# Kernel optimization log

Hardware: AMD Instinct MI355X
Metric: run time of the kernel (lower is better)

The kernel has to match this reference:

```python
import jax, jax.numpy as jnp
import numpy as np

EPS = 1e-15
B, N_PER, D, K, DEG = 64, 1024, 256, 64, 16  # graphs, nodes/graph, feat dim, pools/graph, avg degree


def setup_inputs() -> dict:
    key = jax.random.key(0)
    k1, k2, k3, k4 = jax.random.split(key, 4)
    N = B * N_PER
    E = B * N_PER * DEG
    x = jax.random.normal(k1, (N, D), jnp.float32)
    # edges confined within each graph (block-diagonal batched adjacency)
    rng = np.random.default_rng(0)
    offs = np.repeat(np.arange(B, dtype=np.int64) * N_PER, N_PER * DEG)
    src = rng.integers(0, N_PER, size=E) + offs
    dst = rng.integers(0, N_PER, size=E) + offs
    edge_index = jnp.asarray(np.stack([src, dst], axis=0), dtype=jnp.int32)
    edge_weight = jax.random.uniform(k2, (E,), jnp.float32)
    batch_ptr = jnp.arange(B + 1, dtype=jnp.int32) * N_PER
    W = jax.random.normal(k3, (D, K), jnp.float32) * 0.05  # pooling_net = Linear(D, K)
    b = jnp.zeros((K,), jnp.float32)
    gumbel_noise = jax.random.gumbel(k4, (N, K), jnp.float32)
    return {"x": x, "edge_weight": edge_weight, "W": W, "b": b,
            "gumbel_noise": gumbel_noise, "edge_index": edge_index, "batch_ptr": batch_ptr}


def _stochpool(x, edge_weight, W, b, gumbel_noise, edge_index, batch_ptr):
    N, Dd = x.shape
    nb = batch_ptr.shape[0] - 1          # num graphs
    n = N // nb                          # nodes per graph (equal-sized graphs)
    E = edge_index.shape[1]
    e_per = E // nb                      # edges per graph

    # pooling net + hard gumbel softmax (straight-through, tau=1)
    logits = x @ W + b                   # (N, K)
    y_soft = jax.nn.softmax(logits + gumbel_noise, axis=-1)
    y_hard = jax.nn.one_hot(jnp.argmax(y_soft, axis=-1), W.shape[1], dtype=y_soft.dtype)
    s = jax.lax.stop_gradient(y_hard - y_soft) + y_soft   # (N, K)

    u, v = edge_index[0], edge_index[1]
    graph_of_edge = u // n               # (E,) graph id per edge

    s_b = s.reshape(nb, n, -1)           # (B, n, K)
    x_b = x.reshape(nb, n, Dd)

    # pooled features: s^T x per graph
    out = jnp.einsum('bnk,bnd->bkd', s_b, x_b).reshape(nb * s_b.shape[2], Dd)

    # pooled adjacency: s^T A s per graph, via As = scatter-add over edges
    As = jnp.zeros_like(s).at[u].add(edge_weight[:, None] * s[v])   # (N, K) : (A s)
    out_adj = jnp.einsum('bnk,bnl->bkl', s_b, As.reshape(nb, n, -1))  # (B, K, K)

    # link loss: ||A - S S^T||_F per graph, via Frobenius expansion (no n x n dense)
    sq_A = jax.ops.segment_sum(edge_weight * edge_weight, graph_of_edge, num_segments=nb)
    cross = jax.ops.segment_sum(edge_weight * jnp.sum(s[u] * s[v], axis=-1),
                                graph_of_edge, num_segments=nb)
    StS = jnp.einsum('bnk,bnl->bkl', s_b, s_b)                # (B, K, K)
    sq_SSt = jnp.sum(StS * StS, axis=(1, 2))                  # ||S S^T||_F^2 = ||S^T S||_F^2
    link = jnp.sqrt(jnp.maximum(sq_A - 2.0 * cross + sq_SSt, 0.0))
    link = link / e_per                                       # normalize=True
    link_loss = jnp.mean(link)

    entropy_loss = jnp.mean(jnp.sum(-s * jnp.log(s + EPS), axis=-1))

    Kp = s_b.shape[2]
    batch = jnp.repeat(jnp.arange(nb, dtype=jnp.int32), Kp)
    batch_ptr_out = jnp.arange(0, (nb + 1) * Kp, Kp, dtype=jnp.int32)
    return out, out_adj, link_loss, entropy_loss, batch, batch_ptr_out


def reference(x, edge_weight, W, b, gumbel_noise, edge_index, batch_ptr):
    return _stochpool(x, edge_weight, W, b, gumbel_noise, edge_index, batch_ptr)
```

## Files before the change

### kernel.cpp

```cpp
#include <hip/hip_runtime.h>

#define NN 65536
#define DD 256
#define KK 64
#define NPG 1024

#define OUT_OFF   0
#define ADJ_OFF   1048576
#define LINK_OFF  1310720
#define ENT_OFF   1310721
#define BATCH_OFF 1310722
#define BPTR_OFF  1314818

#define WS_ASSIGN 0
#define WS_S1     262144
#define WS_C      524288
#define WS_SQP    540672
#define WS_CRP    541696
#define WS_ENTP   542720
#define WS_SORT   1048576
#define WS_GOFF   1310720
#define WS_ADJP   1331200
#define WS_NEED   (WS_ADJP + 256 * 4096 * 4)

typedef __bf16 bf16x8 __attribute__((ext_vector_type(8)));
typedef unsigned short u16x8 __attribute__((ext_vector_type(8)));
typedef float f32x4 __attribute__((ext_vector_type(4)));

static __device__ __forceinline__ unsigned short f2bf(float f) {
  unsigned int u = __float_as_uint(f);
  return (unsigned short)((u + 0x7fffu + ((u >> 16) & 1u)) >> 16);
}

__global__ __launch_bounds__(256, 4) void pool_assign_kernel(
    const float* __restrict__ x, const float* __restrict__ Wm,
    const float* __restrict__ bvec, const float* __restrict__ gum,
    int* __restrict__ assign, float* __restrict__ s1g,
    float* __restrict__ entp)
{
  __shared__ unsigned short lds_wt[64 * 264];
  __shared__ float esum[4];
  const int t    = threadIdx.x;
  const int lane = t & 63;
  const int wv   = t >> 6;
  const int q    = lane >> 4;
  const int c    = lane & 15;
  const int nb0  = blockIdx.x << 6;

  #pragma unroll 8
  for (int i = 0; i < 64; ++i) {
    int idx = (i << 8) + t;
    lds_wt[(idx & 63) * 264 + (idx >> 6)] = f2bf(Wm[idx]);
  }

  const int arow = nb0 + (wv << 4) + c;
  const float* xrow = x + (size_t)arow * DD + (q << 3);
  u16x8 afr[8];
  #pragma unroll
  for (int kb = 0; kb < 8; ++kb) {
    float4 u0 = *(const float4*)(xrow + kb * 32);
    float4 u1 = *(const float4*)(xrow + kb * 32 + 4);
    u16x8 af;
    af[0] = f2bf(u0.x); af[1] = f2bf(u0.y); af[2] = f2bf(u0.z); af[3] = f2bf(u0.w);
    af[4] = f2bf(u1.x); af[5] = f2bf(u1.y); af[6] = f2bf(u1.z); af[7] = f2bf(u1.w);
    afr[kb] = af;
  }
  __syncthreads();

  f32x4 acc[4];
  #pragma unroll
  for (int n = 0; n < 4; ++n) acc[n] = (f32x4){0.f, 0.f, 0.f, 0.f};
  #pragma unroll
  for (int n = 0; n < 4; ++n) {
    #pragma unroll
    for (int kb = 0; kb < 8; ++kb) {
      u16x8 bu = *(const u16x8*)(&lds_wt[(n * 16 + c) * 264 + kb * 32 + (q << 3)]);
      acc[n] = __builtin_amdgcn_mfma_f32_16x16x32_bf16(
          __builtin_bit_cast(bf16x8, afr[kb]),
          __builtin_bit_cast(bf16x8, bu), acc[n], 0, 0, 0);
    }
  }

  float bb[4];
  #pragma unroll
  for (int n = 0; n < 4; ++n) bb[n] = bvec[n * 16 + c];
  const int nodeq = nb0 + (wv << 4) + (q << 2);
  float ent = 0.f;
  #pragma unroll
  for (int reg = 0; reg < 4; ++reg) {
    float zz[4];
    #pragma unroll
    for (int n = 0; n < 4; ++n)
      zz[n] = acc[n][reg] + bb[n] + gum[(size_t)(nodeq + reg) * KK + n * 16 + c];
    float m = zz[0]; int a = c;
    #pragma unroll
    for (int n = 1; n < 4; ++n)
      if (zz[n] > m) { m = zz[n]; a = n * 16 + c; }
    #pragma unroll
    for (int mask = 1; mask <= 8; mask <<= 1) {
      float mo = __shfl_xor(m, mask, 64);
      int   ao = __shfl_xor(a, mask, 64);
      if (mo > m || (mo == m && ao < a)) { m = mo; a = ao; }
    }
    float ls = 0.f;
    #pragma unroll
    for (int n = 0; n < 4; ++n) ls += expf(zz[n] - m);
    #pragma unroll
    for (int mask = 1; mask <= 8; mask <<= 1) ls += __shfl_xor(ls, mask, 64);
    if (c == 0) {
      int node = nodeq + reg;
      float p  = 1.0f / ls;
      float s1 = (1.0f - p) + p;
      assign[node] = a;
      s1g[node]    = s1;
      ent += -s1 * logf(s1 + 1e-15f);
    }
  }
  #pragma unroll
  for (int off = 32; off; off >>= 1) ent += __shfl_down(ent, off, 64);
  if (lane == 0) esum[wv] = ent;
  __syncthreads();
  if (t == 0) entp[blockIdx.x] = esum[0] + esum[1] + esum[2] + esum[3];
}

__global__ __launch_bounds__(256) void sort_kernel(
    const int* __restrict__ assign, const float* __restrict__ s1,
    int* __restrict__ sorted, int* __restrict__ goff,
    float* __restrict__ c_out)
{
  __shared__ int hist[64];
  __shared__ int offs[65];
  __shared__ int cursor[64];
  const int t = threadIdx.x;
  const int g = blockIdx.x;
  const int n0 = g << 10;
  if (t < 64) hist[t] = 0;
  __syncthreads();
  int4 av = ((const int4*)(assign + n0))[t];
  atomicAdd(&hist[av.x], 1);
  atomicAdd(&hist[av.y], 1);
  atomicAdd(&hist[av.z], 1);
  atomicAdd(&hist[av.w], 1);
  __syncthreads();
  if (t == 0) {
    int s = 0;
    #pragma unroll
    for (int k = 0; k < 64; ++k) { offs[k] = s; s += hist[k]; }
    offs[64] = s;
  }
  __syncthreads();
  if (t < 64) cursor[t] = offs[t];
  if (t < 65) goff[g * 65 + t] = offs[t];
  __syncthreads();
  int p;
  p = atomicAdd(&cursor[av.x], 1); sorted[n0 + p] = n0 + t * 4 + 0;
  p = atomicAdd(&cursor[av.y], 1); sorted[n0 + p] = n0 + t * 4 + 1;
  p = atomicAdd(&cursor[av.z], 1); sorted[n0 + p] = n0 + t * 4 + 2;
  p = atomicAdd(&cursor[av.w], 1); sorted[n0 + p] = n0 + t * 4 + 3;
  __syncthreads();
  if (t < 64) {
    float cs = 0.f;
    int e = offs[t + 1];
    for (int o = offs[t]; o < e; ++o) {
      float v = s1[sorted[n0 + o]];
      cs += v * v;
    }
    c_out[(g << 6) + t] = cs;
  }
}

__global__ __launch_bounds__(256, 8) void gather_kernel(
    const float* __restrict__ x, const float* __restrict__ s1,
    const int* __restrict__ sorted, const int* __restrict__ goff,
    float* __restrict__ out)
{
  const int t = threadIdx.x;
  const int g = blockIdx.x >> 6;
  const int k = blockIdx.x & 63;
  const int o0 = goff[g * 65 + k];
  const int o1 = goff[g * 65 + k + 1];
  const int* sp = sorted + (g << 10);
  float sum = 0.f;
  int i = o0;
  for (; i + 4 <= o1; i += 4) {
    int n0 = sp[i], n1 = sp[i + 1], n2 = sp[i + 2], n3 = sp[i + 3];
    float w0 = s1[n0], w1 = s1[n1], w2 = s1[n2], w3 = s1[n3];
    float x0 = x[(size_t)n0 * DD + t];
    float x1 = x[(size_t)n1 * DD + t];
    float x2 = x[(size_t)n2 * DD + t];
    float x3 = x[(size_t)n3 * DD + t];
    sum += w0 * x0 + w1 * x1 + w2 * x2 + w3 * x3;
  }
  for (; i < o1; ++i) {
    int n = sp[i];
    sum += s1[n] * x[(size_t)n * DD + t];
  }
  out[((size_t)(g * 64 + k)) * DD + t] = sum;
}

__global__ __launch_bounds__(1024, 2) void edge_kernel(
    const int* __restrict__ src, const int* __restrict__ dst,
    const float* __restrict__ ew, const int* __restrict__ assign,
    const float* __restrict__ s1, float* __restrict__ adj_partial,
    float* __restrict__ sqP, float* __restrict__ crP)
{
  __shared__ float adj[4096];
  __shared__ float redsq[16], redcr[16];
  const int t   = threadIdx.x;
  const int blk = blockIdx.x;
  const int g   = blk >> 2;
  #pragma unroll
  for (int i = 0; i < 4; ++i) adj[i * 1024 + t] = 0.f;
  __syncthreads();
  const int e0 = (g << 14) + ((blk & 3) << 12);
  float sq = 0.f, cr = 0.f;
  #pragma unroll
  for (int i = 0; i < 4; ++i) {
    int e = e0 + i * 1024 + t;
    int u = src[e], v = dst[e];
    float w = ew[e];
    int au = assign[u], av = assign[v];
    float contrib = w * s1[u] * s1[v];
    atomicAdd(&adj[au * 64 + av], contrib);
    sq += w * w;
    if (au == av) cr += contrib;
  }
  #pragma unroll
  for (int off = 32; off; off >>= 1) {
    sq += __shfl_down(sq, off, 64);
    cr += __shfl_down(cr, off, 64);
  }
  if ((t & 63) == 0) { redsq[t >> 6] = sq; redcr[t >> 6] = cr; }
  __syncthreads();
  if (t == 0) {
    float a = 0.f, b2 = 0.f;
    #pragma unroll
    for (int i = 0; i < 16; ++i) { a += redsq[i]; b2 += redcr[i]; }
    sqP[blk] = a;
    crP[blk] = b2;
  }
  float* pp = adj_partial + (size_t)blk * 4096;
  #pragma unroll
  for (int i = 0; i < 4; ++i) pp[i * 1024 + t] = adj[i * 1024 + t];
}

__global__ __launch_bounds__(1024) void adj_combine_kernel(
    const float* __restrict__ adj_partial, float* __restrict__ out_adj)
{
  int idx = blockIdx.x * 1024 + threadIdx.x;
  int g = idx >> 12;
  int cell = idx & 4095;
  const float* p = adj_partial + ((size_t)(g * 4)) * 4096 + cell;
  out_adj[idx] = p[0] + p[4096] + p[8192] + p[12288];
}

__global__ __launch_bounds__(1024, 2) void edge_kernel_atomic(
    const int* __restrict__ src, const int* __restrict__ dst,
    const float* __restrict__ ew, const int* __restrict__ assign,
    const float* __restrict__ s1, float* __restrict__ out_adj,
    float* __restrict__ sqP, float* __restrict__ crP)
{
  __shared__ float adj[4096];
  __shared__ float redsq[16], redcr[16];
  const int t   = threadIdx.x;
  const int blk = blockIdx.x;
  const int g   = blk >> 2;
  #pragma unroll
  for (int i = 0; i < 4; ++i) adj[i * 1024 + t] = 0.f;
  __syncthreads();
  const int e0 = (g << 14) + ((blk & 3) << 12);
  float sq = 0.f, cr = 0.f;
  #pragma unroll
  for (int i = 0; i < 4; ++i) {
    int e = e0 + i * 1024 + t;
    int u = src[e], v = dst[e];
    float w = ew[e];
    int au = assign[u], av = assign[v];
    float contrib = w * s1[u] * s1[v];
    atomicAdd(&adj[au * 64 + av], contrib);
    sq += w * w;
    if (au == av) cr += contrib;
  }
  #pragma unroll
  for (int off = 32; off; off >>= 1) {
    sq += __shfl_down(sq, off, 64);
    cr += __shfl_down(cr, off, 64);
  }
  if ((t & 63) == 0) { redsq[t >> 6] = sq; redcr[t >> 6] = cr; }
  __syncthreads();
  if (t == 0) {
    float a = 0.f, b2 = 0.f;
    #pragma unroll
    for (int i = 0; i < 16; ++i) { a += redsq[i]; b2 += redcr[i]; }
    sqP[blk] = a;
    crP[blk] = b2;
  }
  float* adjg = out_adj + (size_t)g * 4096;
  #pragma unroll
  for (int i = 0; i < 4; ++i)
    atomicAdd(&adjg[i * 1024 + t], adj[i * 1024 + t]);
}

__global__ __launch_bounds__(256) void finalize_kernel(
    const float* __restrict__ c, const float* __restrict__ sqP,
    const float* __restrict__ crP, const float* __restrict__ entp,
    float* __restrict__ out)
{
  __shared__ float esum2[4];
  const int t = threadIdx.x;
  float link = 0.f;
  if (t < 64) {
    const float* cg = c + t * 64;
    float ssq = 0.f;
    #pragma unroll
    for (int k = 0; k < 64; ++k) ssq += cg[k] * cg[k];
    float sq = sqP[4 * t] + sqP[4 * t + 1] + sqP[4 * t + 2] + sqP[4 * t + 3];
    float cr = crP[4 * t] + crP[4 * t + 1] + crP[4 * t + 2] + crP[4 * t + 3];
    float val = sq - 2.0f * cr + ssq;
    link = sqrtf(fmaxf(val, 0.f)) / 16384.0f;
  }
  #pragma unroll
  for (int off = 32; off; off >>= 1) link += __shfl_down(link, off, 64);
  float ent = entp[t] + entp[t + 256] + entp[t + 512] + entp[t + 768];
  #pragma unroll
  for (int off = 32; off; off >>= 1) ent += __shfl_down(ent, off, 64);
  if ((t & 63) == 0) esum2[t >> 6] = ent;
  __syncthreads();
  if (t == 0) {
    out[LINK_OFF] = link / 64.0f;
    out[ENT_OFF]  = (esum2[0] + esum2[1] + esum2[2] + esum2[3]) / (float)NN;
  }
  for (int r = t; r < 4096; r += 256) out[BATCH_OFF + r] = (float)(r >> 6);
  for (int i = t; i < 65; i += 256)   out[BPTR_OFF + i]  = (float)(i << 6);
}

extern "C" void kernel_launch(void* const* d_in, const int* in_sizes, int n_in,
                              void* d_out, int out_size, void* d_ws, size_t ws_size,
                              hipStream_t stream) {
  const float* x    = (const float*)d_in[0];
  const float* ew   = (const float*)d_in[1];
  const float* Wm   = (const float*)d_in[2];
  const float* bvec = (const float*)d_in[3];
  const float* gum  = (const float*)d_in[4];
  const int*   eidx = (const int*)d_in[5];
  float* out = (float*)d_out;
  char*  ws  = (char*)d_ws;

  int*   assign = (int*)(ws + WS_ASSIGN);
  float* s1     = (float*)(ws + WS_S1);
  float* c      = (float*)(ws + WS_C);
  float* sqP    = (float*)(ws + WS_SQP);
  float* crP    = (float*)(ws + WS_CRP);
  float* entp   = (float*)(ws + WS_ENTP);
  int*   sorted = (int*)(ws + WS_SORT);
  int*   goff   = (int*)(ws + WS_GOFF);
  float* adjp   = (float*)(ws + WS_ADJP);

  const int E = in_sizes[1];

  pool_assign_kernel<<<1024, 256, 0, stream>>>(x, Wm, bvec, gum, assign, s1, entp);
  sort_kernel<<<64, 256, 0, stream>>>(assign, s1, sorted, goff, c);
  gather_kernel<<<4096, 256, 0, stream>>>(x, s1, sorted, goff, out + OUT_OFF);
  if (ws_size >= (size_t)WS_NEED) {
    edge_kernel<<<256, 1024, 0, stream>>>(eidx, eidx + E, ew, assign, s1,
                                          adjp, sqP, crP);
    adj_combine_kernel<<<256, 1024, 0, stream>>>(adjp, out + ADJ_OFF);
  } else {
    hipMemsetAsync(out + ADJ_OFF, 0, (size_t)64 * 4096 * 4, stream);
    edge_kernel_atomic<<<256, 1024, 0, stream>>>(eidx, eidx + E, ew, assign, s1,
                                                 out + ADJ_OFF, sqP, crP);
  }
  finalize_kernel<<<1, 256, 0, stream>>>(c, sqP, crP, entp, out);
}
```

Baseline: 60.37 us.

## Fuse gather and edge scatter kernels, pack assign/s1, merge combine with finalize

Packs the cluster assignment and its weight into one int2 per node so the sort, gather and edge passes each do one load instead of two. The feature gather and the edge adjacency scatter now run in a single launch with 5120 blocks, where the first 4096 blocks gather and the rest handle edges. The edge work is split into 1024 blocks of 256 threads with 16 partial adjacencies per graph. Adjacency combine and finalize are merged into one launch. This cuts launch count and lets the two independent phases overlap, at the cost of a larger partial-adjacency workspace and more partials to sum.

```diff
diff --git a/kernel.cpp b/kernel.cpp
--- a/kernel.cpp
+++ b/kernel.cpp
@@ -12,16 +12,15 @@
 #define BATCH_OFF 1310722
 #define BPTR_OFF  1314818
 
-#define WS_ASSIGN 0
-#define WS_S1     262144
+#define WS_S1A    0
 #define WS_C      524288
 #define WS_SQP    540672
-#define WS_CRP    541696
-#define WS_ENTP   542720
-#define WS_SORT   1048576
-#define WS_GOFF   1310720
-#define WS_ADJP   1331200
-#define WS_NEED   (WS_ADJP + 256 * 4096 * 4)
+#define WS_CRP    544768
+#define WS_ENTP   548864
+#define WS_SORTP  552960
+#define WS_GOFF   1077248
+#define WS_ADJP   1093888
+#define WS_NEED   (WS_ADJP + 1024 * 4096 * 4)
 
 typedef __bf16 bf16x8 __attribute__((ext_vector_type(8)));
 typedef unsigned short u16x8 __attribute__((ext_vector_type(8)));
@@ -35,8 +34,7 @@
 __global__ __launch_bounds__(256, 4) void pool_assign_kernel(
     const float* __restrict__ x, const float* __restrict__ Wm,
     const float* __restrict__ bvec, const float* __restrict__ gum,
-    int* __restrict__ assign, float* __restrict__ s1g,
-    float* __restrict__ entp)
+    int2* __restrict__ s1a, float* __restrict__ entp)
 {
   __shared__ unsigned short lds_wt[64 * 264];
   __shared__ float esum[4];
@@ -111,8 +109,7 @@
       int node = nodeq + reg;
       float p  = 1.0f / ls;
       float s1 = (1.0f - p) + p;
-      assign[node] = a;
-      s1g[node]    = s1;
+      s1a[node] = make_int2(a, __float_as_int(s1));
       ent += -s1 * logf(s1 + 1e-15f);
     }
   }
@@ -124,9 +121,8 @@
 }
 
 __global__ __launch_bounds__(256) void sort_kernel(
-    const int* __restrict__ assign, const float* __restrict__ s1,
-    int* __restrict__ sorted, int* __restrict__ goff,
-    float* __restrict__ c_out)
+    const int2* __restrict__ s1a, int2* __restrict__ sortedp,
+    int* __restrict__ goff, float* __restrict__ c_out)
 {
   __shared__ int hist[64];
   __shared__ int offs[65];
@@ -136,11 +132,12 @@
   const int n0 = g << 10;
   if (t < 64) hist[t] = 0;
   __syncthreads();
-  int4 av = ((const int4*)(assign + n0))[t];
-  atomicAdd(&hist[av.x], 1);
-  atomicAdd(&hist[av.y], 1);
-  atomicAdd(&hist[av.z], 1);
-  atomicAdd(&hist[av.w], 1);
+  int4 p01 = ((const int4*)(s1a + n0))[t * 2];
+  int4 p23 = ((const int4*)(s1a + n0))[t * 2 + 1];
+  atomicAdd(&hist[p01.x], 1);
+  atomicAdd(&hist[p01.z], 1);
+  atomicAdd(&hist[p23.x], 1);
+  atomicAdd(&hist[p23.z], 1);
   __syncthreads();
   if (t == 0) {
     int s = 0;
@@ -153,185 +150,236 @@
   if (t < 65) goff[g * 65 + t] = offs[t];
   __syncthreads();
   int p;
-  p = atomicAdd(&cursor[av.x], 1); sorted[n0 + p] = n0 + t * 4 + 0;
-  p = atomicAdd(&cursor[av.y], 1); sorted[n0 + p] = n0 + t * 4 + 1;
-  p = atomicAdd(&cursor[av.z], 1); sorted[n0 + p] = n0 + t * 4 + 2;
-  p = atomicAdd(&cursor[av.w], 1); sorted[n0 + p] = n0 + t * 4 + 3;
+  p = atomicAdd(&cursor[p01.x], 1); sortedp[n0 + p] = make_int2(n0 + t * 4 + 0, p01.y);
+  p = atomicAdd(&cursor[p01.z], 1); sortedp[n0 + p] = make_int2(n0 + t * 4 + 1, p01.w);
+  p = atomicAdd(&cursor[p23.x], 1); sortedp[n0 + p] = make_int2(n0 + t * 4 + 2, p23.y);
+  p = atomicAdd(&cursor[p23.z], 1); sortedp[n0 + p] = make_int2(n0 + t * 4 + 3, p23.w);
   __syncthreads();
   if (t < 64) {
     float cs = 0.f;
     int e = offs[t + 1];
     for (int o = offs[t]; o < e; ++o) {
-      float v = s1[sorted[n0 + o]];
+      float v = __int_as_float(sortedp[n0 + o].y);
       cs += v * v;
     }
     c_out[(g << 6) + t] = cs;
   }
 }
 
+__global__ __launch_bounds__(256, 8) void fuse_ge_kernel(
+    const float* __restrict__ x, const int2* __restrict__ sortedp,
+    const int* __restrict__ goff, const int* __restrict__ src,
+    const int* __restrict__ dst, const float* __restrict__ ew,
+    const int2* __restrict__ s1a, float* __restrict__ out_feat,
+    float* __restrict__ adjp, float* __restrict__ sqP, float* __restrict__ crP)
+{
+  __shared__ float adj[4096];
+  __shared__ float redsq[4], redcr[4];
+  const int t = threadIdx.x;
+  if (blockIdx.x < 4096) {
+    const int g = blockIdx.x >> 6;
+    const int k = blockIdx.x & 63;
+    const int o0 = goff[g * 65 + k];
+    const int o1 = goff[g * 65 + k + 1];
+    const int2* sp = sortedp + (g << 10);
+    float sum = 0.f;
+    int i = o0;
+    for (; i + 4 <= o1; i += 4) {
+      int2 e0 = sp[i], e1 = sp[i + 1], e2 = sp[i + 2], e3 = sp[i + 3];
+      float x0 = x[(size_t)e0.x * DD + t];
+      float x1 = x[(size_t)e1.x * DD + t];
+      float x2 = x[(size_t)e2.x * DD + t];
+      float x3 = x[(size_t)e3.x * DD + t];
+      sum += __int_as_float(e0.y) * x0 + __int_as_float(e1.y) * x1
+           + __int_as_float(e2.y) * x2 + __int_as_float(e3.y) * x3;
+    }
+    for (; i < o1; ++i) {
+      int2 e = sp[i];
+      sum += __int_as_float(e.y) * x[(size_t)e.x * DD + t];
+    }
+    out_feat[((size_t)(g * 64 + k)) * DD + t] = sum;
+  } else {
+    const int blk = blockIdx.x - 4096;
+    const int g   = blk >> 4;
+    #pragma unroll
+    for (int i = 0; i < 16; ++i) adj[i * 256 + t] = 0.f;
+    __syncthreads();
+    const int e0 = blk << 10;
+    float sq = 0.f, cr = 0.f;
+    #pragma unroll
+    for (int i = 0; i < 4; ++i) {
+      int e = e0 + (i << 8) + t;
+      int u = src[e], v = dst[e];
+      float w = ew[e];
+      int2 pu = s1a[u];
+      int2 pv = s1a[v];
+      float contrib = w * __int_as_float(pu.y) * __int_as_float(pv.y);
+      atomicAdd(&adj[pu.x * 64 + pv.x], contrib);
+      sq += w * w;
+      if (pu.x == pv.x) cr += contrib;
+    }
+    #pragma unroll
+    for (int off = 32; off; off >>= 1) {
+      sq += __shfl_down(sq, off, 64);
+      cr += __shfl_down(cr, off, 64);
+    }
+    if ((t & 63) == 0) { redsq[t >> 6] = sq; redcr[t >> 6] = cr; }
+    __syncthreads();
+    if (t == 0) {
+      sqP[blk] = redsq[0] + redsq[1] + redsq[2] + redsq[3];
+      crP[blk] = redcr[0] + redcr[1] + redcr[2] + redcr[3];
+    }
+    float* pp = adjp + (size_t)blk * 4096;
+    #pragma unroll
+    for (int i = 0; i < 16; ++i) pp[i * 256 + t] = adj[i * 256 + t];
+    (void)g;
+  }
+}
+
+__global__ __launch_bounds__(1024) void combine_fin_kernel(
+    const float* __restrict__ adjp, const float* __restrict__ c,
+    const float* __restrict__ sqP, const float* __restrict__ crP,
+    const float* __restrict__ entp, float* __restrict__ out)
+{
+  __shared__ float ered[16];
+  const int t = threadIdx.x;
+  if (blockIdx.x < 256) {
+    int idx = blockIdx.x * 1024 + t;
+    int g = idx >> 12;
+    int cell = idx & 4095;
+    const float* p = adjp + ((size_t)(g * 16)) * 4096 + cell;
+    float s = 0.f;
+    #pragma unroll
+    for (int j = 0; j < 16; ++j) s += p[j * 4096];
+    out[ADJ_OFF + idx] = s;
+    return;
+  }
+  float ent = entp[t];
+  #pragma unroll
+  for (int off = 32; off; off >>= 1) ent += __shfl_down(ent, off, 64);
+  if ((t & 63) == 0) ered[t >> 6] = ent;
+  float link = 0.f;
+  if (t < 64) {
+    const float* cg = c + t * 64;
+    float ssq = 0.f;
+    #pragma unroll
+    for (int k = 0; k < 64; ++k) ssq += cg[k] * cg[k];
+    float sq = 0.f, cr = 0.f;
+    #pragma unroll
+    for (int j = 0; j < 16; ++j) { sq += sqP[t * 16 + j]; cr += crP[t * 16 + j]; }
+    float val = sq - 2.0f * cr + ssq;
+    link = sqrtf(fmaxf(val, 0.f)) / 16384.0f;
+    #pragma unroll
+    for (int off = 32; off; off >>= 1) link += __shfl_down(link, off, 64);
+  }
+  __syncthreads();
+  if (t == 0) {
+    float es = 0.f;
+    #pragma unroll
+    for (int i = 0; i < 16; ++i) es += ered[i];
+    out[LINK_OFF] = link / 64.0f;
+    out[ENT_OFF]  = es / (float)NN;
+  }
+  for (int r = t; r < 4096; r += 1024) out[BATCH_OFF + r] = (float)(r >> 6);
+  if (t < 65) out[BPTR_OFF + t] = (float)(t << 6);
+}
+
+__global__ __launch_bounds__(256) void edge_atomic_kernel(
+    const int* __restrict__ src, const int* __restrict__ dst,
+    const float* __restrict__ ew, const int2* __restrict__ s1a,
+    float* __restrict__ out_adj, float* __restrict__ sqP, float* __restrict__ crP)
+{
+  __shared__ float adj[4096];
+  __shared__ float redsq[4], redcr[4];
+  const int t = threadIdx.x;
+  const int blk = blockIdx.x;
+  const int g = blk >> 4;
+  #pragma unroll
+  for (int i = 0; i < 16; ++i) adj[i * 256 + t] = 0.f;
+  __syncthreads();
+  const int e0 = blk << 10;
+  float sq = 0.f, cr = 0.f;
+  #pragma unroll
+  for (int i = 0; i < 4; ++i) {
+    int e = e0 + (i << 8) + t;
+    int u = src[e], v = dst[e];
+    float w = ew[e];
+    int2 pu = s1a[u];
+    int2 pv = s1a[v];
+    float contrib = w * __int_as_float(pu.y) * __int_as_float(pv.y);
+    atomicAdd(&adj[pu.x * 64 + pv.x], contrib);
+    sq += w * w;
+    if (pu.x == pv.x) cr += contrib;
+  }
+  #pragma unroll
+  for (int off = 32; off; off >>= 1) {
+    sq += __shfl_down(sq, off, 64);
+    cr += __shfl_down(cr, off, 64);
+  }
+  if ((t & 63) == 0) { redsq[t >> 6] = sq; redcr[t >> 6] = cr; }
+  __syncthreads();
+  if (t == 0) {
+    sqP[blk] = redsq[0] + redsq[1] + redsq[2] + redsq[3];
+    crP[blk] = redcr[0] + redcr[1] + redcr[2] + redcr[3];
+  }
+  float* adjg = out_adj + (size_t)g * 4096;
+  #pragma unroll
+  for (int i = 0; i < 16; ++i) atomicAdd(&adjg[i * 256 + t], adj[i * 256 + t]);
+}
+
 __global__ __launch_bounds__(256, 8) void gather_kernel(
-    const float* __restrict__ x, const float* __restrict__ s1,
-    const int* __restrict__ sorted, const int* __restrict__ goff,
-    float* __restrict__ out)
+    const float* __restrict__ x, const int2* __restrict__ sortedp,
+    const int* __restrict__ goff, float* __restrict__ out_feat)
 {
   const int t = threadIdx.x;
   const int g = blockIdx.x >> 6;
   const int k = blockIdx.x & 63;
   const int o0 = goff[g * 65 + k];
   const int o1 = goff[g * 65 + k + 1];
-  const int* sp = sorted + (g << 10);
+  const int2* sp = sortedp + (g << 10);
   float sum = 0.f;
-  int i = o0;
-  for (; i + 4 <= o1; i += 4) {
-    int n0 = sp[i], n1 = sp[i + 1], n2 = sp[i + 2], n3 = sp[i + 3];
-    float w0 = s1[n0], w1 = s1[n1], w2 = s1[n2], w3 = s1[n3];
-    float x0 = x[(size_t)n0 * DD + t];
-    float x1 = x[(size_t)n1 * DD + t];
-    float x2 = x[(size_t)n2 * DD + t];
-    float x3 = x[(size_t)n3 * DD + t];
-    sum += w0 * x0 + w1 * x1 + w2 * x2 + w3 * x3;
-  }
-  for (; i < o1; ++i) {
-    int n = sp[i];
-    sum += s1[n] * x[(size_t)n * DD + t];
-  }
-  out[((size_t)(g * 64 + k)) * DD + t] = sum;
-}
-
-__global__ __launch_bounds__(1024, 2) void edge_kernel(
-    const int* __restrict__ src, const int* __restrict__ dst,
-    const float* __restrict__ ew, const int* __restrict__ assign,
-    const float* __restrict__ s1, float* __restrict__ adj_partial,
-    float* __restrict__ sqP, float* __restrict__ crP)
-{
-  __shared__ float adj[4096];
-  __shared__ float redsq[16], redcr[16];
-  const int t   = threadIdx.x;
-  const int blk = blockIdx.x;
-  const int g   = blk >> 2;
-  #pragma unroll
-  for (int i = 0; i < 4; ++i) adj[i * 1024 + t] = 0.f;
-  __syncthreads();
-  const int e0 = (g << 14) + ((blk & 3) << 12);
-  float sq = 0.f, cr = 0.f;
-  #pragma unroll
-  for (int i = 0; i < 4; ++i) {
-    int e = e0 + i * 1024 + t;
-    int u = src[e], v = dst[e];
-    float w = ew[e];
-    int au = assign[u], av = assign[v];
-    float contrib = w * s1[u] * s1[v];
-    atomicAdd(&adj[au * 64 + av], contrib);
-    sq += w * w;
-    if (au == av) cr += contrib;
-  }
-  #pragma unroll
-  for (int off = 32; off; off >>= 1) {
-    sq += __shfl_down(sq, off, 64);
-    cr += __shfl_down(cr, off, 64);
-  }
-  if ((t & 63) == 0) { redsq[t >> 6] = sq; redcr[t >> 6] = cr; }
-  __syncthreads();
-  if (t == 0) {
-    float a = 0.f, b2 = 0.f;
-    #pragma unroll
-    for (int i = 0; i < 16; ++i) { a += redsq[i]; b2 += redcr[i]; }
-    sqP[blk] = a;
-    crP[blk] = b2;
-  }
-  float* pp = adj_partial + (size_t)blk * 4096;
-  #pragma unroll
-  for (int i = 0; i < 4; ++i) pp[i * 1024 + t] = adj[i * 1024 + t];
-}
-
-__global__ __launch_bounds__(1024) void adj_combine_kernel(
-    const float* __restrict__ adj_partial, float* __restrict__ out_adj)
-{
-  int idx = blockIdx.x * 1024 + threadIdx.x;
-  int g = idx >> 12;
-  int cell = idx & 4095;
-  const float* p = adj_partial + ((size_t)(g * 4)) * 4096 + cell;
-  out_adj[idx] = p[0] + p[4096] + p[8192] + p[12288];
-}
-
-__global__ __launch_bounds__(1024, 2) void edge_kernel_atomic(
-    const int* __restrict__ src, const int* __restrict__ dst,
-    const float* __restrict__ ew, const int* __restrict__ assign,
-    const float* __restrict__ s1, float* __restrict__ out_adj,
-    float* __restrict__ sqP, float* __restrict__ crP)
-{
-  __shared__ float adj[4096];
-  __shared__ float redsq[16], redcr[16];
-  const int t   = threadIdx.x;
-  const int blk = blockIdx.x;
-  const int g   = blk >> 2;
-  #pragma unroll
-  for (int i = 0; i < 4; ++i) adj[i * 1024 + t] = 0.f;
-  __syncthreads();
-  const int e0 = (g << 14) + ((blk & 3) << 12);
-  float sq = 0.f, cr = 0.f;
-  #pragma unroll
-  for (int i = 0; i < 4; ++i) {
-    int e = e0 + i * 1024 + t;
-    int u = src[e], v = dst[e];
-    float w = ew[e];
-    int au = assign[u], av = assign[v];
-    float contrib = w * s1[u] * s1[v];
-    atomicAdd(&adj[au * 64 + av], contrib);
-    sq += w * w;
-    if (au == av) cr += contrib;
-  }
-  #pragma unroll
-  for (int off = 32; off; off >>= 1) {
-    sq += __shfl_down(sq, off, 64);
-    cr += __shfl_down(cr, off, 64);
-  }
-  if ((t & 63) == 0) { redsq[t >> 6] = sq; redcr[t >> 6] = cr; }
-  __syncthreads();
-  if (t == 0) {
-    float a = 0.f, b2 = 0.f;
-    #pragma unroll
-    for (int i = 0; i < 16; ++i) { a += redsq[i]; b2 += redcr[i]; }
-    sqP[blk] = a;
-    crP[blk] = b2;
-  }
-  float* adjg = out_adj + (size_t)g * 4096;
-  #pragma unroll
-  for (int i = 0; i < 4; ++i)
-    atomicAdd(&adjg[i * 1024 + t], adj[i * 1024 + t]);
-}
-
-__global__ __launch_bounds__(256) void finalize_kernel(
+  for (int i = o0; i < o1; ++i) {
+    int2 e = sp[i];
+    sum += __int_as_float(e.y) * x[(size_t)e.x * DD + t];
+  }
+  out_feat[((size_t)(g * 64 + k)) * DD + t] = sum;
+}
+
+__global__ __launch_bounds__(1024) void finalize_only_kernel(
     const float* __restrict__ c, const float* __restrict__ sqP,
     const float* __restrict__ crP, const float* __restrict__ entp,
     float* __restrict__ out)
 {
-  __shared__ float esum2[4];
-  const int t = threadIdx.x;
+  __shared__ float ered[16];
+  const int t = threadIdx.x;
+  float ent = entp[t];
+  #pragma unroll
+  for (int off = 32; off; off >>= 1) ent += __shfl_down(ent, off, 64);
+  if ((t & 63) == 0) ered[t >> 6] = ent;
   float link = 0.f;
   if (t < 64) {
     const float* cg = c + t * 64;
     float ssq = 0.f;
     #pragma unroll
     for (int k = 0; k < 64; ++k) ssq += cg[k] * cg[k];
-    float sq = sqP[4 * t] + sqP[4 * t + 1] + sqP[4 * t + 2] + sqP[4 * t + 3];
-    float cr = crP[4 * t] + crP[4 * t + 1] + crP[4 * t + 2] + crP[4 * t + 3];
+    float sq = 0.f, cr = 0.f;
+    #pragma unroll
+    for (int j = 0; j < 16; ++j) { sq += sqP[t * 16 + j]; cr += crP[t * 16 + j]; }
     float val = sq - 2.0f * cr + ssq;
     link = sqrtf(fmaxf(val, 0.f)) / 16384.0f;
-  }
-  #pragma unroll
-  for (int off = 32; off; off >>= 1) link += __shfl_down(link, off, 64);
-  float ent = entp[t] + entp[t + 256] + entp[t + 512] + entp[t + 768];
-  #pragma unroll
-  for (int off = 32; off; off >>= 1) ent += __shfl_down(ent, off, 64);
-  if ((t & 63) == 0) esum2[t >> 6] = ent;
+    #pragma unroll
+    for (int off = 32; off; off >>= 1) link += __shfl_down(link, off, 64);
+  }
   __syncthreads();
   if (t == 0) {
+    float es = 0.f;
+    #pragma unroll
+    for (int i = 0; i < 16; ++i) es += ered[i];
     out[LINK_OFF] = link / 64.0f;
-    out[ENT_OFF]  = (esum2[0] + esum2[1] + esum2[2] + esum2[3]) / (float)NN;
-  }
-  for (int r = t; r < 4096; r += 256) out[BATCH_OFF + r] = (float)(r >> 6);
-  for (int i = t; i < 65; i += 256)   out[BPTR_OFF + i]  = (float)(i << 6);
+    out[ENT_OFF]  = es / (float)NN;
+  }
+  for (int r = t; r < 4096; r += 1024) out[BATCH_OFF + r] = (float)(r >> 6);
+  if (t < 65) out[BPTR_OFF + t] = (float)(t << 6);
 }
 
 extern "C" void kernel_launch(void* const* d_in, const int* in_sizes, int n_in,
@@ -346,29 +394,28 @@
   float* out = (float*)d_out;
   char*  ws  = (char*)d_ws;
 
-  int*   assign = (int*)(ws + WS_ASSIGN);
-  float* s1     = (float*)(ws + WS_S1);
-  float* c      = (float*)(ws + WS_C);
-  float* sqP    = (float*)(ws + WS_SQP);
-  float* crP    = (float*)(ws + WS_CRP);
-  float* entp   = (float*)(ws + WS_ENTP);
-  int*   sorted = (int*)(ws + WS_SORT);
-  int*   goff   = (int*)(ws + WS_GOFF);
-  float* adjp   = (float*)(ws + WS_ADJP);
+  int2*  s1a     = (int2*)(ws + WS_S1A);
+  float* c       = (float*)(ws + WS_C);
+  float* sqP     = (float*)(ws + WS_SQP);
+  float* crP     = (float*)(ws + WS_CRP);
+  float* entp    = (float*)(ws + WS_ENTP);
+  int2*  sortedp = (int2*)(ws + WS_SORTP);
+  int*   goff    = (int*)(ws + WS_GOFF);
+  float* adjp    = (float*)(ws + WS_ADJP);
 
   const int E = in_sizes[1];
 
-  pool_assign_kernel<<<1024, 256, 0, stream>>>(x, Wm, bvec, gum, assign, s1, entp);
-  sort_kernel<<<64, 256, 0, stream>>>(assign, s1, sorted, goff, c);
-  gather_kernel<<<4096, 256, 0, stream>>>(x, s1, sorted, goff, out + OUT_OFF);
+  pool_assign_kernel<<<1024, 256, 0, stream>>>(x, Wm, bvec, gum, s1a, entp);
+  sort_kernel<<<64, 256, 0, stream>>>(s1a, sortedp, goff, c);
   if (ws_size >= (size_t)WS_NEED) {
-    edge_kernel<<<256, 1024, 0, stream>>>(eidx, eidx + E, ew, assign, s1,
-                                          adjp, sqP, crP);
-    adj_combine_kernel<<<256, 1024, 0, stream>>>(adjp, out + ADJ_OFF);
+    fuse_ge_kernel<<<5120, 256, 0, stream>>>(x, sortedp, goff, eidx, eidx + E,
+                                             ew, s1a, out + OUT_OFF, adjp, sqP, crP);
+    combine_fin_kernel<<<257, 1024, 0, stream>>>(adjp, c, sqP, crP, entp, out);
   } else {
     hipMemsetAsync(out + ADJ_OFF, 0, (size_t)64 * 4096 * 4, stream);
-    edge_kernel_atomic<<<256, 1024, 0, stream>>>(eidx, eidx + E, ew, assign, s1,
+    gather_kernel<<<4096, 256, 0, stream>>>(x, sortedp, goff, out + OUT_OFF);
+    edge_atomic_kernel<<<1024, 256, 0, stream>>>(eidx, eidx + E, ew, s1a,
                                                  out + ADJ_OFF, sqP, crP);
-  }
-  finalize_kernel<<<1, 256, 0, stream>>>(c, sqP, crP, entp, out);
-}
+    finalize_only_kernel<<<1, 1024, 0, stream>>>(c, sqP, crP, entp, out);
+  }
+}
```

After: 60.52 us. Within noise of the previous version (+0.3%).
